# Kernel optimization log

Measured on AMD Instinct MI355X. Metric: run time of the kernel, lower is better.

## Reference

```python
import jax, jax.numpy as jnp
import numpy as np

L, D, N = 4096, 1024, 16  # seq_len, d_model, hiddens_per_input


def setup_inputs() -> dict:
    key = jax.random.key(0)
    ks = jax.random.split(key, 9)
    x = jax.random.normal(ks[0], (L, D), dtype=jnp.float32)
    # Delta param (pre-softplus); softplus(Delta) > 0 is the discretization step
    Delta = jax.random.normal(ks[1], (D,), dtype=jnp.float32)
    # A stored as (re, im); default scheme uses A_re = -1 (stable), theta in [0, 2pi)
    A_re = -(0.5 + 0.5 * jax.random.uniform(ks[2], (D, N), dtype=jnp.float32))
    A_im = jax.random.uniform(ks[3], (D, N), dtype=jnp.float32) * 2.0 * jnp.pi
    scale = 1.0 / jnp.sqrt(jnp.float32(D))  # matrix_init: randn / sqrt(shape[0])
    B_re = jax.random.normal(ks[4], (D, N), dtype=jnp.float32) * scale
    B_im = jax.random.normal(ks[5], (D, N), dtype=jnp.float32) * scale
    C_re = jax.random.normal(ks[6], (D, N), dtype=jnp.float32) * scale
    C_im = jax.random.normal(ks[7], (D, N), dtype=jnp.float32) * scale
    D_param = jax.random.normal(ks[8], (D,), dtype=jnp.float32) * scale
    return {"x": x, "Delta": Delta, "A_re": A_re, "A_im": A_im,
            "B_re": B_re, "B_im": B_im, "C_re": C_re, "C_im": C_im,
            "D_param": D_param}


def _binary_operator_diag(q_i, q_j):
    """Associative op for diagonal linear recurrence h_j = A_j h_{j-1} + b_j."""
    A_i, b_i = q_i
    A_j, b_j = q_j
    return (A_j * A_i, A_j * b_i + b_j)


def reference(x, Delta, A_re, A_im, B_re, B_im, C_re, C_im, D_param):
    Bc = B_re + 1j * B_im                      # (D, N) complex
    Cc = C_re + 1j * C_im                      # (D, N) complex
    Ac = A_re + 1j * A_im                      # (D, N) complex
    dt = jax.nn.softplus(Delta)                # (D,)
    # shared_Delta=True branch: Lambda = exp(dt[:, None] * A), repeated over L
    Lam = jnp.exp(dt[:, None] * Ac)            # (D, N) complex
    Lambda_elements = jnp.broadcast_to(Lam[None, :, :], (x.shape[0], *Lam.shape))
    # Bu = einsum('D, D N, L D -> L D N', dt, B, x)
    Bu_elements = jnp.einsum('D,DN,LD->LDN', dt.astype(Bc.dtype), Bc,
                             x.astype(Bc.dtype))
    _, hidden_states = jax.lax.associative_scan(
        _binary_operator_diag, (Lambda_elements, Bu_elements))  # (L, D, N)
    out = jnp.einsum('LDN,DN->LD', hidden_states, Cc) + D_param[None, :] * x
    return out.real
```

## Files before the change

kernel.cpp:

```cpp
#include <hip/hip_runtime.h>
#include <math.h>

constexpr int L  = 4096;
constexpr int D  = 1024;
constexpr int N  = 16;
constexpr int NC = 64;
constexpr int T  = L / NC;
constexpr int DG = 64;
constexpr int G  = D / DG;

__device__ __forceinline__ float softplus_f(float v) {
    return fmaxf(v, 0.0f) + log1pf(expf(-fabsf(v)));
}

__device__ __forceinline__ void lam_fast(float ar, float ai, float dt,
                                         float& lr, float& li) {
    float e = __expf(ar * dt);
    float s, c;
    __sincosf(ai * dt, &s, &c);
    lr = e * c;
    li = e * s;
}

__global__ __launch_bounds__(256, 4) void k_local(
    const float* __restrict__ x,
    const float* __restrict__ Delta,
    const float* __restrict__ A_re, const float* __restrict__ A_im,
    float2* __restrict__ s2)
{
    __shared__ float xs[T * DG];
    const int c  = blockIdx.x >> 4;
    const int dg = blockIdx.x & 15;
    const int t  = threadIdx.x;

    const float* xg = x + (size_t)c * T * D + dg * DG;
    #pragma unroll
    for (int it = 0; it < 4; ++it) {
        int f = t * 4 + it * 1024;
        int row = f >> 6, col = f & 63;
        *(float4*)&xs[row * DG + col] =
            *(const float4*)(xg + (size_t)row * D + col);
    }

    const int q = t & 3, dl = t >> 2;
    const int d = dg * DG + dl;
    const float dt = softplus_f(Delta[d]);
    float Lr[4], Li[4];
    {
        float4 a0 = *(const float4*)(A_re + d * N + q * 4);
        float4 a1 = *(const float4*)(A_im + d * N + q * 4);
        const float ar[4] = {a0.x, a0.y, a0.z, a0.w};
        const float ai[4] = {a1.x, a1.y, a1.z, a1.w};
        #pragma unroll
        for (int j = 0; j < 4; ++j) lam_fast(ar[j], ai[j], dt, Lr[j], Li[j]);
    }
    __syncthreads();

    float gr[4] = {0, 0, 0, 0}, gi[4] = {0, 0, 0, 0};
    #pragma unroll
    for (int i = 0; i < T; ++i) {
        float xv = xs[i * DG + dl];
        #pragma unroll
        for (int j = 0; j < 4; ++j) {
            float t2 = fmaf(-Li[j], gi[j], xv);
            float nr = fmaf(Lr[j], gr[j], t2);
            gi[j] = fmaf(Lr[j], gi[j], Li[j] * gr[j]);
            gr[j] = nr;
        }
    }
    #pragma unroll
    for (int j = 0; j < 4; ++j)
        s2[((size_t)c * N + q * 4 + j) * D + d] = make_float2(gr[j], gi[j]);
}

__global__ __launch_bounds__(64) void k_scan(
    const float* __restrict__ Delta,
    const float* __restrict__ A_re, const float* __restrict__ A_im,
    float2* __restrict__ s2)
{
    const int tid = blockIdx.x * 64 + threadIdx.x;
    const int d = tid & (D - 1);
    const int n = tid >> 10;

    const float dt = softplus_f(Delta[d]);
    float Lr, Li;
    lam_fast(A_re[d * N + n], A_im[d * N + n], dt, Lr, Li);
    #pragma unroll
    for (int k = 0; k < 6; ++k) {
        float nr = Lr * Lr - Li * Li;
        Li = 2.0f * Lr * Li;
        Lr = nr;
    }

    float cr = 0.0f, ci = 0.0f;
    #pragma unroll
    for (int c0 = 0; c0 < NC; c0 += 32) {
        float2 sv[32];
        #pragma unroll
        for (int u = 0; u < 32; ++u)
            sv[u] = s2[(size_t)(c0 + u) * (N * D) + tid];
        #pragma unroll
        for (int u = 0; u < 32; ++u) {
            s2[(size_t)(c0 + u) * (N * D) + tid] = make_float2(cr, ci);
            float nr = fmaf(Lr, cr, fmaf(-Li, ci, sv[u].x));
            ci = fmaf(Lr, ci, fmaf(Li, cr, sv[u].y));
            cr = nr;
        }
    }
}

__global__ __launch_bounds__(256, 4) void k_out(
    const float* __restrict__ x,
    const float* __restrict__ Delta,
    const float* __restrict__ A_re, const float* __restrict__ A_im,
    const float* __restrict__ B_re, const float* __restrict__ B_im,
    const float* __restrict__ C_re, const float* __restrict__ C_im,
    const float* __restrict__ Dp,
    const float2* __restrict__ s2,
    float* __restrict__ out)
{
    __shared__ float xs[T * DG];
    const int c  = blockIdx.x >> 4;
    const int dg = blockIdx.x & 15;
    const int t  = threadIdx.x;

    const float* xg = x + (size_t)c * T * D + dg * DG;
    #pragma unroll
    for (int it = 0; it < 4; ++it) {
        int f = t * 4 + it * 1024;
        int row = f >> 6, col = f & 63;
        *(float4*)&xs[row * DG + col] =
            *(const float4*)(xg + (size_t)row * D + col);
    }

    const int q = t & 3, dl = t >> 2;
    const int d = dg * DG + dl;
    const float dt  = softplus_f(Delta[d]);
    const float dpv = Dp[d];

    float Lr[4], Li[4], Cr[4], Ci[4], gr[4], gi[4];
    {
        const int pidx = d * N + q * 4;
        float4 a0 = *(const float4*)(A_re + pidx);
        float4 a1 = *(const float4*)(A_im + pidx);
        float4 b0 = *(const float4*)(B_re + pidx);
        float4 b1 = *(const float4*)(B_im + pidx);
        float4 c0 = *(const float4*)(C_re + pidx);
        float4 c1 = *(const float4*)(C_im + pidx);
        const float ar[4] = {a0.x, a0.y, a0.z, a0.w};
        const float ai[4] = {a1.x, a1.y, a1.z, a1.w};
        const float br[4] = {b0.x, b0.y, b0.z, b0.w};
        const float bi[4] = {b1.x, b1.y, b1.z, b1.w};
        const float crr[4] = {c0.x, c0.y, c0.z, c0.w};
        const float cii[4] = {c1.x, c1.y, c1.z, c1.w};
        #pragma unroll
        for (int j = 0; j < 4; ++j) {
            lam_fast(ar[j], ai[j], dt, Lr[j], Li[j]);
            Cr[j] = dt * (crr[j] * br[j] - cii[j] * bi[j]);
            Ci[j] = dt * (crr[j] * bi[j] + cii[j] * br[j]);
        }
    }
    #pragma unroll
    for (int j = 0; j < 4; ++j) {
        float2 cv = s2[((size_t)c * N + q * 4 + j) * D + d];
        gr[j] = cv.x; gi[j] = cv.y;
    }
    float* og = out + (size_t)c * T * D + dg * DG;
    __syncthreads();

    #pragma unroll
    for (int ib = 0; ib < T / 4; ++ib) {
        float keep = 0.0f;
        #pragma unroll
        for (int u = 0; u < 4; ++u) {
            int i = ib * 4 + u;
            float xv = xs[i * DG + dl];
            float acc = 0.0f;
            #pragma unroll
            for (int j = 0; j < 4; ++j) {
                float t2 = fmaf(-Li[j], gi[j], xv);
                float nr = fmaf(Lr[j], gr[j], t2);
                gi[j] = fmaf(Lr[j], gi[j], Li[j] * gr[j]);
                gr[j] = nr;
                acc = fmaf(Cr[j], gr[j], acc);
                acc = fmaf(-Ci[j], gi[j], acc);
            }
            acc += __shfl_xor(acc, 1);
            acc += __shfl_xor(acc, 2);
            acc = fmaf(dpv, xv, acc);
            keep = (q == u) ? acc : keep;
        }
        og[(size_t)(ib * 4 + q) * D + dl] = keep;
    }
}

extern "C" void kernel_launch(void* const* d_in, const int* in_sizes, int n_in,
                              void* d_out, int out_size, void* d_ws, size_t ws_size,
                              hipStream_t stream) {
    const float* x     = (const float*)d_in[0];
    const float* Delta = (const float*)d_in[1];
    const float* A_re  = (const float*)d_in[2];
    const float* A_im  = (const float*)d_in[3];
    const float* B_re  = (const float*)d_in[4];
    const float* B_im  = (const float*)d_in[5];
    const float* C_re  = (const float*)d_in[6];
    const float* C_im  = (const float*)d_in[7];
    const float* Dp    = (const float*)d_in[8];
    float* out = (float*)d_out;
    float2* s2 = (float2*)d_ws;

    k_local<<<NC * G, 256, 0, stream>>>(x, Delta, A_re, A_im, s2);
    k_scan<<<(N * D) / 64, 64, 0, stream>>>(Delta, A_re, A_im, s2);
    k_out<<<NC * G, 256, 0, stream>>>(x, Delta, A_re, A_im, B_re, B_im,
                                      C_re, C_im, Dp, s2, out);
}
```

Baseline: 108.5 us.

## Fold chunk-carry scan into output kernel and drop separate scan launch

Removes the sequential k_scan kernel. Each k_out block now computes its own incoming carry by scanning the local chunk states of all preceding chunks, using Lambda^T obtained by repeated squaring. The workspace layout changes to a per-(chunk, d) float4-packed format so each thread reads its states with vector loads, and the block index mapping in k_out is swapped so that consecutive blocks share a d-group. This saves a kernel launch and a round-trip write of carries, but adds redundant work: later chunks re-scan up to 63 prior states, which is quadratic in chunk count and causes load imbalance across blocks.

After: 125.9 us. +16.1%, slower.

```diff
diff --git a/kernel.cpp b/kernel.cpp
--- a/kernel.cpp
+++ b/kernel.cpp
@@ -22,11 +22,12 @@
     li = e * s;
 }
 
+
 __global__ __launch_bounds__(256, 4) void k_local(
     const float* __restrict__ x,
     const float* __restrict__ Delta,
     const float* __restrict__ A_re, const float* __restrict__ A_im,
-    float2* __restrict__ s2)
+    float4* __restrict__ s4)
 {
     __shared__ float xs[T * DG];
     const int c  = blockIdx.x >> 4;
@@ -68,45 +69,9 @@
             gr[j] = nr;
         }
     }
-    #pragma unroll
-    for (int j = 0; j < 4; ++j)
-        s2[((size_t)c * N + q * 4 + j) * D + d] = make_float2(gr[j], gi[j]);
-}
-
-__global__ __launch_bounds__(64) void k_scan(
-    const float* __restrict__ Delta,
-    const float* __restrict__ A_re, const float* __restrict__ A_im,
-    float2* __restrict__ s2)
-{
-    const int tid = blockIdx.x * 64 + threadIdx.x;
-    const int d = tid & (D - 1);
-    const int n = tid >> 10;
-
-    const float dt = softplus_f(Delta[d]);
-    float Lr, Li;
-    lam_fast(A_re[d * N + n], A_im[d * N + n], dt, Lr, Li);
-    #pragma unroll
-    for (int k = 0; k < 6; ++k) {
-        float nr = Lr * Lr - Li * Li;
-        Li = 2.0f * Lr * Li;
-        Lr = nr;
-    }
-
-    float cr = 0.0f, ci = 0.0f;
-    #pragma unroll
-    for (int c0 = 0; c0 < NC; c0 += 32) {
-        float2 sv[32];
-        #pragma unroll
-        for (int u = 0; u < 32; ++u)
-            sv[u] = s2[(size_t)(c0 + u) * (N * D) + tid];
-        #pragma unroll
-        for (int u = 0; u < 32; ++u) {
-            s2[(size_t)(c0 + u) * (N * D) + tid] = make_float2(cr, ci);
-            float nr = fmaf(Lr, cr, fmaf(-Li, ci, sv[u].x));
-            ci = fmaf(Lr, ci, fmaf(Li, cr, sv[u].y));
-            cr = nr;
-        }
-    }
+    float4* dst = s4 + ((size_t)c * D + d) * 8 + q * 2;
+    dst[0] = make_float4(gr[0], gi[0], gr[1], gi[1]);
+    dst[1] = make_float4(gr[2], gi[2], gr[3], gi[3]);
 }
 
 __global__ __launch_bounds__(256, 4) void k_out(
@@ -116,12 +81,12 @@
     const float* __restrict__ B_re, const float* __restrict__ B_im,
     const float* __restrict__ C_re, const float* __restrict__ C_im,
     const float* __restrict__ Dp,
-    const float2* __restrict__ s2,
+    const float4* __restrict__ s4,
     float* __restrict__ out)
 {
     __shared__ float xs[T * DG];
-    const int c  = blockIdx.x >> 4;
-    const int dg = blockIdx.x & 15;
+    const int c  = blockIdx.x & 63;
+    const int dg = blockIdx.x >> 6;
     const int t  = threadIdx.x;
 
     const float* xg = x + (size_t)c * T * D + dg * DG;
@@ -138,7 +103,7 @@
     const float dt  = softplus_f(Delta[d]);
     const float dpv = Dp[d];
 
-    float Lr[4], Li[4], Cr[4], Ci[4], gr[4], gi[4];
+    float Lr[4], Li[4], Tr[4], Ti[4], Cr[4], Ci[4];
     {
         const int pidx = d * N + q * 4;
         float4 a0 = *(const float4*)(A_re + pidx);
@@ -156,15 +121,54 @@
         #pragma unroll
         for (int j = 0; j < 4; ++j) {
             lam_fast(ar[j], ai[j], dt, Lr[j], Li[j]);
+            float tr = Lr[j], ti = Li[j];
+            #pragma unroll
+            for (int k = 0; k < 6; ++k) {
+                float nr = tr * tr - ti * ti;
+                ti = 2.0f * tr * ti;
+                tr = nr;
+            }
+            Tr[j] = tr; Ti[j] = ti;
             Cr[j] = dt * (crr[j] * br[j] - cii[j] * bi[j]);
             Ci[j] = dt * (crr[j] * bi[j] + cii[j] * br[j]);
         }
     }
-    #pragma unroll
-    for (int j = 0; j < 4; ++j) {
-        float2 cv = s2[((size_t)c * N + q * 4 + j) * D + d];
-        gr[j] = cv.x; gi[j] = cv.y;
-    }
+
+    float gr[4] = {0, 0, 0, 0}, gi[4] = {0, 0, 0, 0};
+    const float4* sp = s4 + (size_t)d * 8 + q * 2;
+    int p = 0;
+    for (; p + 4 <= c; p += 4) {
+        float4 s0[4], s1[4];
+        #pragma unroll
+        for (int u = 0; u < 4; ++u) {
+            const float4* src = sp + (size_t)(p + u) * D * 8;
+            s0[u] = src[0]; s1[u] = src[1];
+        }
+        #pragma unroll
+        for (int u = 0; u < 4; ++u) {
+            const float sx[4] = {s0[u].x, s0[u].z, s1[u].x, s1[u].z};
+            const float sy[4] = {s0[u].y, s0[u].w, s1[u].y, s1[u].w};
+            #pragma unroll
+            for (int j = 0; j < 4; ++j) {
+                float nr = fmaf(Tr[j], gr[j], fmaf(-Ti[j], gi[j], sx[j]));
+                gi[j] = fmaf(Tr[j], gi[j], fmaf(Ti[j], gr[j], sy[j]));
+                gr[j] = nr;
+            }
+        }
+    }
+    for (; p < c; ++p) {
+        const float4* src = sp + (size_t)p * D * 8;
+        float4 s0 = src[0], s1 = src[1];
+        const float sx[4] = {s0.x, s0.z, s1.x, s1.z};
+        const float sy[4] = {s0.y, s0.w, s1.y, s1.w};
+        #pragma unroll
+        for (int j = 0; j < 4; ++j) {
+            float nr = fmaf(Tr[j], gr[j], fmaf(-Ti[j], gi[j], sx[j]));
+            gi[j] = fmaf(Tr[j], gi[j], fmaf(Ti[j], gr[j], sy[j]));
+            gr[j] = nr;
+        }
+    }
+
     float* og = out + (size_t)c * T * D + dg * DG;
     __syncthreads();
 
@@ -207,10 +211,9 @@
     const float* C_im  = (const float*)d_in[7];
     const float* Dp    = (const float*)d_in[8];
     float* out = (float*)d_out;
-    float2* s2 = (float2*)d_ws;
-
-    k_local<<<NC * G, 256, 0, stream>>>(x, Delta, A_re, A_im, s2);
-    k_scan<<<(N * D) / 64, 64, 0, stream>>>(Delta, A_re, A_im, s2);
+    float4* s4 = (float4*)d_ws;
+
+    k_local<<<NC * G, 256, 0, stream>>>(x, Delta, A_re, A_im, s4);
     k_out<<<NC * G, 256, 0, stream>>>(x, Delta, A_re, A_im, B_re, B_im,
-                                      C_re, C_im, Dp, s2, out);
-}
+                                      C_re, C_im, Dp, s4, out);
+}
```
